# Kernel optimization log

Hardware: AMD Instinct MI355X
Metric: run time of the kernel (lower is better)

## Reference

```python
import jax, jax.numpy as jnp
import numpy as np

D_MODEL = 1024
N_HEADS = 16
EPS = 1e-6


def setup_inputs() -> dict:
    key = jax.random.key(0)
    k1, k2, k3 = jax.random.split(key, 3)
    B, T, D = 2, 2048, D_MODEL
    x = jax.random.normal(k1, (B, T, D), dtype=jnp.float32)
    # learned params
    norm_weight = jnp.ones((D,), dtype=jnp.float32)
    qkv_w = jax.random.normal(k2, (3 * D, D), dtype=jnp.float32) * (1.0 / np.sqrt(D))
    out_w = jax.random.normal(k3, (D, D), dtype=jnp.float32) * (1.0 / np.sqrt(D))
    return {"x": x, "norm_weight": norm_weight, "qkv_w": qkv_w, "out_w": out_w}


def reference(x, norm_weight, qkv_w, out_w):
    B, T, D = x.shape
    H = N_HEADS
    d = D // H
    # RMSNorm
    ms = jnp.mean(x * x, axis=-1, keepdims=True)
    xn = x * jax.lax.rsqrt(ms + EPS) * norm_weight
    # QKV projection (Linear, no bias): y = x @ W^T
    qkv = jnp.einsum('btd,ed->bte', xn, qkv_w)  # (B,T,3D)
    q, k, v = jnp.split(qkv, 3, axis=-1)
    q = q.reshape(B, T, H, d)
    k = k.reshape(B, T, H, d)
    v = v.reshape(B, T, H, d)
    # scores (B,H,T,T) with causal mask
    scores = jnp.einsum('bqhd,bkhd->bhqk', q, k) / np.sqrt(d).astype(np.float32)
    causal = jnp.tril(jnp.ones((T, T), dtype=bool))
    scores = jnp.where(causal[None, None], scores, -jnp.inf)
    probs = jax.nn.softmax(scores, axis=-1)
    ctx = jnp.einsum('bhqk,bkhd->bqhd', probs, v)  # (B,T,H,d)
    out = ctx.reshape(B, T, D)
    out = jnp.einsum('btd,ed->bte', out, out_w)
    return out
```

## Files before the change

kernel.cpp:

```cpp
#include <hip/hip_runtime.h>
#include <stdint.h>

#define B_SZ 2
#define T_SZ 2048
#define DMODEL 1024
#define HCNT 16
#define HD 64
#define MROWS (B_SZ * T_SZ)

typedef __attribute__((ext_vector_type(8))) __bf16 bf16x8;
typedef __attribute__((ext_vector_type(4))) __bf16 bf16x4;
typedef __attribute__((ext_vector_type(4))) float f32x4;
typedef __attribute__((ext_vector_type(8))) unsigned short u16x8;

__device__ __forceinline__ unsigned short f2bf(float f) {
  union { float f; uint32_t u; } v; v.f = f;
  uint32_t u = v.u;
  u += 0x7fffu + ((u >> 16) & 1u);
  return (unsigned short)(u >> 16);
}

__device__ __forceinline__ float fexp2(float x) {
#if __has_builtin(__builtin_amdgcn_exp2f)
  return __builtin_amdgcn_exp2f(x);
#else
  return exp2f(x);
#endif
}

__device__ __forceinline__ void gld_lds16(const void* g, void* l) {
  __builtin_amdgcn_global_load_lds((__attribute__((address_space(1))) void*)(uintptr_t)g,
                                   (__attribute__((address_space(3))) void*)l, 16, 0, 0);
}

__global__ __launch_bounds__(256)
void cvt_all(const float* __restrict__ qkv_w, const float* __restrict__ out_w,
             unsigned short* __restrict__ dst) {
  int i = blockIdx.x * 256 + threadIdx.x;
  const int n1 = 3 * DMODEL * DMODEL / 4;
  float4 v = (i < n1) ? ((const float4*)qkv_w)[i] : ((const float4*)out_w)[i - n1];
  ushort4 o;
  o.x = f2bf(v.x); o.y = f2bf(v.y); o.z = f2bf(v.z); o.w = f2bf(v.w);
  ((ushort4*)dst)[i] = o;
}

__global__ __launch_bounds__(256)
void rmsnorm_bf16(const float* __restrict__ x, const float* __restrict__ w,
                  unsigned short* __restrict__ xn) {
  const int row = blockIdx.x;
  const int t = threadIdx.x;
  float4 v = ((const float4*)(x + (size_t)row * DMODEL))[t];
  float ss = v.x * v.x + v.y * v.y + v.z * v.z + v.w * v.w;
#pragma unroll
  for (int o = 1; o < 64; o <<= 1) ss += __shfl_xor(ss, o, 64);
  __shared__ float red[4];
  if ((t & 63) == 0) red[t >> 6] = ss;
  __syncthreads();
  float tot = red[0] + red[1] + red[2] + red[3];
  float scale = rsqrtf(tot * (1.0f / (float)DMODEL) + 1e-6f);
  float4 wv = ((const float4*)w)[t];
  ushort4 o;
  o.x = f2bf(v.x * scale * wv.x);
  o.y = f2bf(v.y * scale * wv.y);
  o.z = f2bf(v.z * scale * wv.z);
  o.w = f2bf(v.w * scale * wv.w);
  ((ushort4*)(xn + (size_t)row * DMODEL))[t] = o;
}

__device__ __forceinline__ void stage128x32(const unsigned short* g, int ldg,
                                            unsigned short* lds, int wave, int lane) {
#pragma unroll
  for (int i = 0; i < 2; ++i) {
    const unsigned short* gp = g + (size_t)(i * 64 + wave * 16 + (lane >> 2)) * ldg + (lane & 3) * 8;
    gld_lds16(gp, lds + i * 2048 + wave * 512);
  }
}

template <int F32OUT>
__global__ __launch_bounds__(256, 2)
void gemm_bt(const unsigned short* __restrict__ A, const unsigned short* __restrict__ B,
             void* __restrict__ Cv, int M, int N, int K, int nbx) {
  __shared__ __align__(16) unsigned short As[2][128 * 32];
  __shared__ __align__(16) unsigned short Bs[2][128 * 32];
  const int t = threadIdx.x, wave = t >> 6, lane = t & 63;
  const int cpx = gridDim.x >> 3;
  const int swz = (blockIdx.x & 7) * cpx + (blockIdx.x >> 3);
  const int m0 = (swz / nbx) * 128, n0 = (swz % nbx) * 128;
  const int wr = wave >> 1, wc = wave & 1;
  f32x4 acc[4][4] = {};
  const int nk = K >> 5;
  stage128x32(A + (size_t)m0 * K, K, As[0], wave, lane);
  stage128x32(B + (size_t)n0 * K, K, Bs[0], wave, lane);
  __syncthreads();
  int buf = 0;
  for (int kt = 0; kt < nk; ++kt) {
    if (kt + 1 < nk) {
      stage128x32(A + (size_t)m0 * K + (kt + 1) * 32, K, As[buf ^ 1], wave, lane);
      stage128x32(B + (size_t)n0 * K + (kt + 1) * 32, K, Bs[buf ^ 1], wave, lane);
    }
    bf16x8 af[4], bfr[4];
#pragma unroll
    for (int mi = 0; mi < 4; ++mi)
      af[mi] = *(const bf16x8*)&As[buf][(wr * 64 + mi * 16 + (lane & 15)) * 32 + (lane >> 4) * 8];
#pragma unroll
    for (int ni = 0; ni < 4; ++ni)
      bfr[ni] = *(const bf16x8*)&Bs[buf][(wc * 64 + ni * 16 + (lane & 15)) * 32 + (lane >> 4) * 8];
#pragma unroll
    for (int mi = 0; mi < 4; ++mi)
#pragma unroll
      for (int ni = 0; ni < 4; ++ni)
        acc[mi][ni] = __builtin_amdgcn_mfma_f32_16x16x32_bf16(af[mi], bfr[ni], acc[mi][ni], 0, 0, 0);
    __syncthreads();
    buf ^= 1;
  }
  const int cr = (lane >> 4) * 4, cc = lane & 15;
#pragma unroll
  for (int mi = 0; mi < 4; ++mi)
#pragma unroll
    for (int ni = 0; ni < 4; ++ni) {
      int row = m0 + wr * 64 + mi * 16 + cr;
      int col = n0 + wc * 64 + ni * 16 + cc;
      if (F32OUT) {
        float* C = (float*)Cv;
#pragma unroll
        for (int r = 0; r < 4; ++r) C[(size_t)(row + r) * N + col] = acc[mi][ni][r];
      } else {
        unsigned short* C = (unsigned short*)Cv;
#pragma unroll
        for (int r = 0; r < 4; ++r) C[(size_t)(row + r) * N + col] = f2bf(acc[mi][ni][r]);
      }
    }
}

__global__ __launch_bounds__(256, 2)
void attn_causal(const unsigned short* __restrict__ qkv, unsigned short* __restrict__ ctx) {
  __shared__ __align__(16) unsigned short Ks[2][128 * 64];
  __shared__ __align__(16) unsigned short Vt[2][64 * 72];
  __shared__ __align__(16) unsigned short Pl[4][32 * 72];
  const int tid = threadIdx.x, wave = tid >> 6, lane = tid & 63;
  const int id = blockIdx.x;
  const int bh = (id & 7) + 8 * ((id >> 3) & 3);
  const int p = id >> 5;
  const int qt = (p < 8) ? (15 - p) : (p - 8);
  const int b = bh >> 4, h = bh & 15;
  const int q0 = qt * 128 + wave * 32;
  const size_t base = (size_t)b * T_SZ * 3 * DMODEL;
  const int koffK = DMODEL + h * HD;
  const int koffV = 2 * DMODEL + h * HD;
  const int nit = qt + 1;
  const int c = lane & 15, qg = lane >> 4;

  const float QSC = 0.125f * 1.4426950408889634f;
  bf16x8 aq[2][2];
#pragma unroll
  for (int mi = 0; mi < 2; ++mi)
#pragma unroll
    for (int kk = 0; kk < 2; ++kk) {
      int q = q0 + mi * 16 + c;
      bf16x8 f = *(const bf16x8*)(qkv + base + (size_t)q * 3 * DMODEL + h * HD + kk * 32 + qg * 8);
#pragma unroll
      for (int j = 0; j < 8; ++j) f[j] = (__bf16)((float)f[j] * QSC);
      aq[mi][kk] = f;
    }

  float mst[2] = {-3e38f, -3e38f}, lst[2] = {0.f, 0.f};
  f32x4 aco[2][4];
#pragma unroll
  for (int mi = 0; mi < 2; ++mi)
#pragma unroll
    for (int nd = 0; nd < 4; ++nd)
#pragma unroll
      for (int r = 0; r < 4; ++r) aco[mi][nd][r] = 0.f;

  const int kr = tid >> 3;
  const int kc = tid & 7;

  auto stageK = [&](int kb, int bufi) {
#pragma unroll
    for (int i = 0; i < 4; ++i) {
      int row = i * 32 + kr;
      gld_lds16(qkv + base + (size_t)(kb + row) * 3 * DMODEL + koffK + ((kc ^ (row & 7)) << 3),
                &Ks[bufi][i * 2048 + (wave << 9)]);
    }
  };
  auto loadV = [&](int kb, u16x8* v) {
#pragma unroll
    for (int i = 0; i < 4; ++i)
      v[i] = *(const u16x8*)(qkv + base + (size_t)(kb + i * 32 + kr) * 3 * DMODEL + koffV + kc * 8);
  };
  auto writeV = [&](const u16x8* v) {
#pragma unroll
    for (int i = 0; i < 4; ++i) {
      int ch = i >> 1;
      int kv = (i & 1) * 32 + kr;
#pragma unroll
      for (int j = 0; j < 8; ++j) {
        int dd = kc * 8 + j;
        int f = kc ^ j;
        Vt[ch][dd * 72 + ((((kv >> 3) ^ f) << 3) | (kv & 7))] = v[i][j];
      }
    }
  };

  auto computeTile = [&](int kb, int kbuf) {
    f32x4 s[8][2] = {};
    __builtin_amdgcn_s_setprio(1);
#pragma unroll
    for (int kk = 0; kk < 2; ++kk) {
      bf16x8 bk[8];
#pragma unroll
      for (int ni = 0; ni < 8; ++ni) {
        int row = ni * 16 + c;
        int crd = kk * 4 + qg;
        bk[ni] = *(const bf16x8*)&Ks[kbuf][row * 64 + ((crd ^ (row & 7)) << 3)];
      }
#pragma unroll
      for (int ni = 0; ni < 8; ++ni)
#pragma unroll
        for (int mi = 0; mi < 2; ++mi)
          s[ni][mi] = __builtin_amdgcn_mfma_f32_16x16x32_bf16(bk[ni], aq[mi][kk], s[ni][mi], 0, 0, 0);
    }
    __builtin_amdgcn_s_setprio(0);
    if (kb + 127 > q0) {
#pragma unroll
      for (int ni = 0; ni < 8; ++ni)
#pragma unroll
        for (int mi = 0; mi < 2; ++mi)
#pragma unroll
          for (int r = 0; r < 4; ++r) {
            int kg = kb + ni * 16 + qg * 4 + r;
            int qq = q0 + mi * 16 + c;
            if (kg > qq) s[ni][mi][r] = -1e30f;
          }
    }
#pragma unroll
    for (int mi = 0; mi < 2; ++mi) {
      float rm = -3e38f;
#pragma unroll
      for (int ni = 0; ni < 8; ++ni)
#pragma unroll
        for (int r = 0; r < 4; ++r) rm = fmaxf(rm, s[ni][mi][r]);
      rm = fmaxf(rm, __shfl_xor(rm, 16, 64));
      rm = fmaxf(rm, __shfl_xor(rm, 32, 64));
      float mo = mst[mi];
      float mn = mo;
      if (__any(rm > mo + 11.5f)) {
        mn = fmaxf(mo, rm);
        float corr = fexp2(mo - mn);
        lst[mi] *= corr;
        mst[mi] = mn;
#pragma unroll
        for (int r = 0; r < 4; ++r) {
          float cr = __shfl(corr, qg * 20 + r, 64);
#pragma unroll
          for (int nd = 0; nd < 4; ++nd) aco[mi][nd][r] *= cr;
        }
      }
      float rs = 0.f;
#pragma unroll
      for (int ni = 0; ni < 8; ++ni)
#pragma unroll
        for (int r = 0; r < 4; ++r) {
          float pv = fexp2(s[ni][mi][r] - mn);
          s[ni][mi][r] = pv;
          rs += pv;
        }
      rs += __shfl_xor(rs, 16, 64);
      rs += __shfl_xor(rs, 32, 64);
      lst[mi] += rs;
    }
    unsigned short* P = Pl[wave];
#pragma unroll
    for (int ch = 0; ch < 2; ++ch) {
      if (ch == 1) {
        asm volatile("s_waitcnt lgkmcnt(0)" ::: "memory");
        __builtin_amdgcn_sched_barrier(0);
      }
#pragma unroll
      for (int n2 = 0; n2 < 4; ++n2) {
        int ni = ch * 4 + n2;
#pragma unroll
        for (int mi = 0; mi < 2; ++mi) {
          bf16x4 pk;
#pragma unroll
          for (int r = 0; r < 4; ++r) pk[r] = (__bf16)s[ni][mi][r];
          *(bf16x4*)&P[(mi * 16 + c) * 72 + n2 * 16 + qg * 4] = pk;
        }
      }
      __builtin_amdgcn_s_setprio(1);
#pragma unroll
      for (int kk = 0; kk < 2; ++kk) {
        bf16x8 pa[2], bv[4];
#pragma unroll
        for (int mi = 0; mi < 2; ++mi)
          pa[mi] = *(const bf16x8*)&P[(mi * 16 + c) * 72 + kk * 32 + qg * 8];
#pragma unroll
        for (int nd = 0; nd < 4; ++nd) {
          int dd = nd * 16 + c;
          int f = ((dd >> 3) ^ dd) & 7;
          int crd = kk * 4 + qg;
          bv[nd] = *(const bf16x8*)&Vt[ch][dd * 72 + ((crd ^ f) << 3)];
        }
#pragma unroll
        for (int mi = 0; mi < 2; ++mi)
#pragma unroll
          for (int nd = 0; nd < 4; ++nd)
            aco[mi][nd] = __builtin_amdgcn_mfma_f32_16x16x32_bf16(pa[mi], bv[nd], aco[mi][nd], 0, 0, 0);
      }
      __builtin_amdgcn_s_setprio(0);
    }
  };

  stageK(0, 0);
  u16x8 v0[4];
  loadV(0, v0);
  __syncthreads();
  writeV(v0);
  __syncthreads();
  int kbuf = 0;
  for (int t = 0; t < nit; ++t) {
    const int kb = t * 128;
    const bool hn = (t + 1 < nit);
    u16x8 vn[4];
    if (hn) { stageK(kb + 128, kbuf ^ 1); loadV(kb + 128, vn); }
    computeTile(kb, kbuf);
    __syncthreads();
    if (hn) writeV(vn);
    __syncthreads();
    kbuf ^= 1;
  }

  unsigned short* outp = ctx + (size_t)b * T_SZ * DMODEL + h * HD;
#pragma unroll
  for (int mi = 0; mi < 2; ++mi) {
    float linv = 1.f / lst[mi];
#pragma unroll
    for (int r = 0; r < 4; ++r) {
      float inv = __shfl(linv, qg * 20 + r, 64);
      int q = q0 + mi * 16 + qg * 4 + r;
#pragma unroll
      for (int nd = 0; nd < 4; ++nd)
        outp[(size_t)q * DMODEL + nd * 16 + c] = f2bf(aco[mi][nd][r] * inv);
    }
  }
}

extern "C" void kernel_launch(void* const* d_in, const int* in_sizes, int n_in,
                              void* d_out, int out_size, void* d_ws, size_t ws_size,
                              hipStream_t stream) {
  const float* x = (const float*)d_in[0];
  const float* nw = (const float*)d_in[1];
  const float* qkv_w = (const float*)d_in[2];
  const float* out_w = (const float*)d_in[3];
  float* out = (float*)d_out;

  unsigned short* ws = (unsigned short*)d_ws;
  unsigned short* xn = ws;
  unsigned short* qkvw = xn + (size_t)MROWS * DMODEL;
  unsigned short* outw = qkvw + (size_t)3 * DMODEL * DMODEL;
  unsigned short* qkv = outw + (size_t)DMODEL * DMODEL;
  unsigned short* ctx = qkv + (size_t)MROWS * 3 * DMODEL;

  cvt_all<<<dim3(4096), dim3(256), 0, stream>>>(qkv_w, out_w, qkvw);
  rmsnorm_bf16<<<dim3(MROWS), dim3(256), 0, stream>>>(x, nw, xn);
  gemm_bt<0><<<dim3(768), dim3(256), 0, stream>>>(xn, qkvw, qkv, MROWS, 3 * DMODEL, DMODEL, 24);
  attn_causal<<<dim3(512), dim3(256), 0, stream>>>(qkv, ctx);
  gemm_bt<1><<<dim3(256), dim3(256), 0, stream>>>(ctx, outw, out, MROWS, DMODEL, DMODEL, 8);
}
```

Before: 121.1 us.

## Pair causal query tiles per attention block and widen GEMM K-tile

The attention kernel now launches 256 blocks of 512 threads. Each block handles two query tiles, p and 15-p, for one batch-head, so every block does a balanced amount of causal work and shares its K/V staging across both tiles. Each wave now owns 16 rows from each tile. V is double-buffered in LDS, which drops one barrier per iteration, and the two masked diagonal tiles are handled separately. Separately, the GEMM stages a 64-wide K slice per iteration to halve its loop trips and barriers, at the cost of double the LDS.

```diff
diff --git a/kernel.cpp b/kernel.cpp
--- a/kernel.cpp
+++ b/kernel.cpp
@@ -67,11 +67,12 @@
   ((ushort4*)(xn + (size_t)row * DMODEL))[t] = o;
 }
 
-__device__ __forceinline__ void stage128x32(const unsigned short* g, int ldg,
-                                            unsigned short* lds, int wave, int lane) {
-#pragma unroll
-  for (int i = 0; i < 2; ++i) {
-    const unsigned short* gp = g + (size_t)(i * 64 + wave * 16 + (lane >> 2)) * ldg + (lane & 3) * 8;
+__device__ __forceinline__ void stage128x64(const unsigned short* g, int ldg,
+                                            unsigned short* lds, int tid) {
+  const int wave = tid >> 6;
+#pragma unroll
+  for (int i = 0; i < 4; ++i) {
+    const unsigned short* gp = g + (size_t)(i * 32 + (tid >> 3)) * ldg + (tid & 7) * 8;
     gld_lds16(gp, lds + i * 2048 + wave * 512);
   }
 }
@@ -80,46 +81,50 @@
 __global__ __launch_bounds__(256, 2)
 void gemm_bt(const unsigned short* __restrict__ A, const unsigned short* __restrict__ B,
              void* __restrict__ Cv, int M, int N, int K, int nbx) {
-  __shared__ __align__(16) unsigned short As[2][128 * 32];
-  __shared__ __align__(16) unsigned short Bs[2][128 * 32];
+  __shared__ __align__(16) unsigned short As[2][128 * 64];
+  __shared__ __align__(16) unsigned short Bs[2][128 * 64];
   const int t = threadIdx.x, wave = t >> 6, lane = t & 63;
   const int cpx = gridDim.x >> 3;
   const int swz = (blockIdx.x & 7) * cpx + (blockIdx.x >> 3);
   const int m0 = (swz / nbx) * 128, n0 = (swz % nbx) * 128;
   const int wr = wave >> 1, wc = wave & 1;
+  const int c = lane & 15, qg = lane >> 4;
   f32x4 acc[4][4] = {};
-  const int nk = K >> 5;
-  stage128x32(A + (size_t)m0 * K, K, As[0], wave, lane);
-  stage128x32(B + (size_t)n0 * K, K, Bs[0], wave, lane);
+  const int nk = K >> 6;
+  stage128x64(A + (size_t)m0 * K, K, As[0], t);
+  stage128x64(B + (size_t)n0 * K, K, Bs[0], t);
   __syncthreads();
   int buf = 0;
   for (int kt = 0; kt < nk; ++kt) {
     if (kt + 1 < nk) {
-      stage128x32(A + (size_t)m0 * K + (kt + 1) * 32, K, As[buf ^ 1], wave, lane);
-      stage128x32(B + (size_t)n0 * K + (kt + 1) * 32, K, Bs[buf ^ 1], wave, lane);
-    }
-    bf16x8 af[4], bfr[4];
-#pragma unroll
-    for (int mi = 0; mi < 4; ++mi)
-      af[mi] = *(const bf16x8*)&As[buf][(wr * 64 + mi * 16 + (lane & 15)) * 32 + (lane >> 4) * 8];
-#pragma unroll
-    for (int ni = 0; ni < 4; ++ni)
-      bfr[ni] = *(const bf16x8*)&Bs[buf][(wc * 64 + ni * 16 + (lane & 15)) * 32 + (lane >> 4) * 8];
-#pragma unroll
-    for (int mi = 0; mi < 4; ++mi)
+      stage128x64(A + (size_t)m0 * K + (kt + 1) * 64, K, As[buf ^ 1], t);
+      stage128x64(B + (size_t)n0 * K + (kt + 1) * 64, K, Bs[buf ^ 1], t);
+    }
+#pragma unroll
+    for (int kk = 0; kk < 2; ++kk) {
+      bf16x8 af[4], bfr[4];
+#pragma unroll
+      for (int mi = 0; mi < 4; ++mi)
+        af[mi] = *(const bf16x8*)&As[buf][(wr * 64 + mi * 16 + c) * 64 + kk * 32 + qg * 8];
 #pragma unroll
       for (int ni = 0; ni < 4; ++ni)
-        acc[mi][ni] = __builtin_amdgcn_mfma_f32_16x16x32_bf16(af[mi], bfr[ni], acc[mi][ni], 0, 0, 0);
+        bfr[ni] = *(const bf16x8*)&Bs[buf][(wc * 64 + ni * 16 + c) * 64 + kk * 32 + qg * 8];
+#pragma unroll
+      for (int mi = 0; mi < 4; ++mi)
+#pragma unroll
+        for (int ni = 0; ni < 4; ++ni)
+          acc[mi][ni] = __builtin_amdgcn_mfma_f32_16x16x32_bf16(af[mi], bfr[ni], acc[mi][ni], 0, 0, 0);
+    }
     __syncthreads();
     buf ^= 1;
   }
-  const int cr = (lane >> 4) * 4, cc = lane & 15;
+  const int cr = qg * 4;
 #pragma unroll
   for (int mi = 0; mi < 4; ++mi)
 #pragma unroll
     for (int ni = 0; ni < 4; ++ni) {
       int row = m0 + wr * 64 + mi * 16 + cr;
-      int col = n0 + wc * 64 + ni * 16 + cc;
+      int col = n0 + wc * 64 + ni * 16 + c;
       if (F32OUT) {
         float* C = (float*)Cv;
 #pragma unroll
@@ -132,23 +137,23 @@
     }
 }
 
-__global__ __launch_bounds__(256, 2)
+__global__ __launch_bounds__(512, 2)
 void attn_causal(const unsigned short* __restrict__ qkv, unsigned short* __restrict__ ctx) {
   __shared__ __align__(16) unsigned short Ks[2][128 * 64];
-  __shared__ __align__(16) unsigned short Vt[2][64 * 72];
-  __shared__ __align__(16) unsigned short Pl[4][32 * 72];
+  __shared__ __align__(16) unsigned short Vt[2][2][64 * 72];
+  __shared__ __align__(16) unsigned short Pl[8][32 * 136];
   const int tid = threadIdx.x, wave = tid >> 6, lane = tid & 63;
   const int id = blockIdx.x;
-  const int bh = (id & 7) + 8 * ((id >> 3) & 3);
-  const int p = id >> 5;
-  const int qt = (p < 8) ? (15 - p) : (p - 8);
+  const int bh = (id & 7) | ((id >> 6) << 3);
+  const int p = (id >> 3) & 7;
   const int b = bh >> 4, h = bh & 15;
-  const int q0 = qt * 128 + wave * 32;
+  const int q0a = p * 128 + wave * 16;
+  const int q0b = (15 - p) * 128 + wave * 16;
+  const int nit = 16 - p;
+  const int c = lane & 15, qg = lane >> 4;
   const size_t base = (size_t)b * T_SZ * 3 * DMODEL;
   const int koffK = DMODEL + h * HD;
   const int koffV = 2 * DMODEL + h * HD;
-  const int nit = qt + 1;
-  const int c = lane & 15, qg = lane >> 4;
 
   const float QSC = 0.125f * 1.4426950408889634f;
   bf16x8 aq[2][2];
@@ -156,7 +161,7 @@
   for (int mi = 0; mi < 2; ++mi)
 #pragma unroll
     for (int kk = 0; kk < 2; ++kk) {
-      int q = q0 + mi * 16 + c;
+      int q = (mi ? q0b : q0a) + c;
       bf16x8 f = *(const bf16x8*)(qkv + base + (size_t)q * 3 * DMODEL + h * HD + kk * 32 + qg * 8);
 #pragma unroll
       for (int j = 0; j < 8; ++j) f[j] = (__bf16)((float)f[j] * QSC);
@@ -172,37 +177,69 @@
 #pragma unroll
       for (int r = 0; r < 4; ++r) aco[mi][nd][r] = 0.f;
 
-  const int kr = tid >> 3;
-  const int kc = tid & 7;
-
   auto stageK = [&](int kb, int bufi) {
 #pragma unroll
-    for (int i = 0; i < 4; ++i) {
-      int row = i * 32 + kr;
-      gld_lds16(qkv + base + (size_t)(kb + row) * 3 * DMODEL + koffK + ((kc ^ (row & 7)) << 3),
-                &Ks[bufi][i * 2048 + (wave << 9)]);
+    for (int i = 0; i < 2; ++i) {
+      int row = i * 64 + (tid >> 3);
+      gld_lds16(qkv + base + (size_t)(kb + row) * 3 * DMODEL + koffK + (((tid & 7) ^ (row & 7)) << 3),
+                &Ks[bufi][i * 4096 + (wave << 9)]);
     }
   };
   auto loadV = [&](int kb, u16x8* v) {
 #pragma unroll
-    for (int i = 0; i < 4; ++i)
-      v[i] = *(const u16x8*)(qkv + base + (size_t)(kb + i * 32 + kr) * 3 * DMODEL + koffV + kc * 8);
-  };
-  auto writeV = [&](const u16x8* v) {
-#pragma unroll
-    for (int i = 0; i < 4; ++i) {
-      int ch = i >> 1;
-      int kv = (i & 1) * 32 + kr;
+    for (int i = 0; i < 2; ++i)
+      v[i] = *(const u16x8*)(qkv + base + (size_t)(kb + i * 64 + (tid >> 3)) * 3 * DMODEL + koffV + (tid & 7) * 8);
+  };
+  auto writeV = [&](int bufi, const u16x8* v) {
+#pragma unroll
+    for (int i = 0; i < 2; ++i) {
+      int kv = tid >> 3;
 #pragma unroll
       for (int j = 0; j < 8; ++j) {
-        int dd = kc * 8 + j;
-        int f = kc ^ j;
-        Vt[ch][dd * 72 + ((((kv >> 3) ^ f) << 3) | (kv & 7))] = v[i][j];
-      }
-    }
-  };
-
-  auto computeTile = [&](int kb, int kbuf) {
+        int dd = (tid & 7) * 8 + j;
+        int f = (tid & 7) ^ j;
+        Vt[bufi][i][dd * 72 + ((((kv >> 3) ^ f) << 3) | (kv & 7))] = v[i][j];
+      }
+    }
+  };
+
+  auto softmaxRow = [&](int mi, f32x4 s[8][2]) {
+    float rm = -3e38f;
+#pragma unroll
+    for (int ni = 0; ni < 8; ++ni)
+#pragma unroll
+      for (int r = 0; r < 4; ++r) rm = fmaxf(rm, s[ni][mi][r]);
+    rm = fmaxf(rm, __shfl_xor(rm, 16, 64));
+    rm = fmaxf(rm, __shfl_xor(rm, 32, 64));
+    float mo = mst[mi];
+    float mn = mo;
+    if (__any(rm > mo + 11.5f)) {
+      mn = fmaxf(mo, rm);
+      float corr = fexp2(mo - mn);
+      lst[mi] *= corr;
+      mst[mi] = mn;
+#pragma unroll
+      for (int r = 0; r < 4; ++r) {
+        float cr = __shfl(corr, qg * 20 + r, 64);
+#pragma unroll
+        for (int nd = 0; nd < 4; ++nd) aco[mi][nd][r] *= cr;
+      }
+    }
+    float rs = 0.f;
+#pragma unroll
+    for (int ni = 0; ni < 8; ++ni)
+#pragma unroll
+      for (int r = 0; r < 4; ++r) {
+        float pv = fexp2(s[ni][mi][r] - mn);
+        s[ni][mi][r] = pv;
+        rs += pv;
+      }
+    rs += __shfl_xor(rs, 16, 64);
+    rs += __shfl_xor(rs, 32, 64);
+    lst[mi] += rs;
+  };
+
+  auto computeTile = [&](int kb, int kbuf, bool both, bool maskA, bool maskB) {
     f32x4 s[8][2] = {};
     __builtin_amdgcn_s_setprio(1);
 #pragma unroll
@@ -216,116 +253,91 @@
       }
 #pragma unroll
       for (int ni = 0; ni < 8; ++ni)
-#pragma unroll
-        for (int mi = 0; mi < 2; ++mi)
-          s[ni][mi] = __builtin_amdgcn_mfma_f32_16x16x32_bf16(bk[ni], aq[mi][kk], s[ni][mi], 0, 0, 0);
+        s[ni][1] = __builtin_amdgcn_mfma_f32_16x16x32_bf16(bk[ni], aq[1][kk], s[ni][1], 0, 0, 0);
+      if (both)
+#pragma unroll
+        for (int ni = 0; ni < 8; ++ni)
+          s[ni][0] = __builtin_amdgcn_mfma_f32_16x16x32_bf16(bk[ni], aq[0][kk], s[ni][0], 0, 0, 0);
     }
     __builtin_amdgcn_s_setprio(0);
-    if (kb + 127 > q0) {
+    if (maskB) {
 #pragma unroll
       for (int ni = 0; ni < 8; ++ni)
 #pragma unroll
-        for (int mi = 0; mi < 2; ++mi)
-#pragma unroll
-          for (int r = 0; r < 4; ++r) {
-            int kg = kb + ni * 16 + qg * 4 + r;
-            int qq = q0 + mi * 16 + c;
-            if (kg > qq) s[ni][mi][r] = -1e30f;
-          }
-    }
-#pragma unroll
-    for (int mi = 0; mi < 2; ++mi) {
-      float rm = -3e38f;
+        for (int r = 0; r < 4; ++r) {
+          int kg = kb + ni * 16 + qg * 4 + r;
+          if (kg > q0b + c) s[ni][1][r] = -1e30f;
+        }
+    }
+    if (both && maskA) {
 #pragma unroll
       for (int ni = 0; ni < 8; ++ni)
 #pragma unroll
-        for (int r = 0; r < 4; ++r) rm = fmaxf(rm, s[ni][mi][r]);
-      rm = fmaxf(rm, __shfl_xor(rm, 16, 64));
-      rm = fmaxf(rm, __shfl_xor(rm, 32, 64));
-      float mo = mst[mi];
-      float mn = mo;
-      if (__any(rm > mo + 11.5f)) {
-        mn = fmaxf(mo, rm);
-        float corr = fexp2(mo - mn);
-        lst[mi] *= corr;
-        mst[mi] = mn;
-#pragma unroll
         for (int r = 0; r < 4; ++r) {
-          float cr = __shfl(corr, qg * 20 + r, 64);
-#pragma unroll
-          for (int nd = 0; nd < 4; ++nd) aco[mi][nd][r] *= cr;
+          int kg = kb + ni * 16 + qg * 4 + r;
+          if (kg > q0a + c) s[ni][0][r] = -1e30f;
         }
-      }
-      float rs = 0.f;
-#pragma unroll
-      for (int ni = 0; ni < 8; ++ni)
-#pragma unroll
-        for (int r = 0; r < 4; ++r) {
-          float pv = fexp2(s[ni][mi][r] - mn);
-          s[ni][mi][r] = pv;
-          rs += pv;
-        }
-      rs += __shfl_xor(rs, 16, 64);
-      rs += __shfl_xor(rs, 32, 64);
-      lst[mi] += rs;
-    }
+    }
+    softmaxRow(1, s);
+    if (both) softmaxRow(0, s);
     unsigned short* P = Pl[wave];
 #pragma unroll
-    for (int ch = 0; ch < 2; ++ch) {
-      if (ch == 1) {
-        asm volatile("s_waitcnt lgkmcnt(0)" ::: "memory");
-        __builtin_amdgcn_sched_barrier(0);
-      }
-#pragma unroll
-      for (int n2 = 0; n2 < 4; ++n2) {
-        int ni = ch * 4 + n2;
-#pragma unroll
-        for (int mi = 0; mi < 2; ++mi) {
-          bf16x4 pk;
-#pragma unroll
-          for (int r = 0; r < 4; ++r) pk[r] = (__bf16)s[ni][mi][r];
-          *(bf16x4*)&P[(mi * 16 + c) * 72 + n2 * 16 + qg * 4] = pk;
-        }
-      }
-      __builtin_amdgcn_s_setprio(1);
+    for (int ni = 0; ni < 8; ++ni) {
+      {
+        bf16x4 pk;
+#pragma unroll
+        for (int r = 0; r < 4; ++r) pk[r] = (__bf16)s[ni][1][r];
+        *(bf16x4*)&P[(16 + c) * 136 + ni * 16 + qg * 4] = pk;
+      }
+      if (both) {
+        bf16x4 pk;
+#pragma unroll
+        for (int r = 0; r < 4; ++r) pk[r] = (__bf16)s[ni][0][r];
+        *(bf16x4*)&P[c * 136 + ni * 16 + qg * 4] = pk;
+      }
+    }
+    __builtin_amdgcn_s_setprio(1);
+#pragma unroll
+    for (int ch = 0; ch < 2; ++ch)
 #pragma unroll
       for (int kk = 0; kk < 2; ++kk) {
-        bf16x8 pa[2], bv[4];
-#pragma unroll
-        for (int mi = 0; mi < 2; ++mi)
-          pa[mi] = *(const bf16x8*)&P[(mi * 16 + c) * 72 + kk * 32 + qg * 8];
+        bf16x8 bv[4];
 #pragma unroll
         for (int nd = 0; nd < 4; ++nd) {
           int dd = nd * 16 + c;
           int f = ((dd >> 3) ^ dd) & 7;
           int crd = kk * 4 + qg;
-          bv[nd] = *(const bf16x8*)&Vt[ch][dd * 72 + ((crd ^ f) << 3)];
+          bv[nd] = *(const bf16x8*)&Vt[kbuf][ch][dd * 72 + ((crd ^ f) << 3)];
         }
-#pragma unroll
-        for (int mi = 0; mi < 2; ++mi)
+        bf16x8 pa1 = *(const bf16x8*)&P[(16 + c) * 136 + ch * 64 + kk * 32 + qg * 8];
+#pragma unroll
+        for (int nd = 0; nd < 4; ++nd)
+          aco[1][nd] = __builtin_amdgcn_mfma_f32_16x16x32_bf16(pa1, bv[nd], aco[1][nd], 0, 0, 0);
+        if (both) {
+          bf16x8 pa0 = *(const bf16x8*)&P[c * 136 + ch * 64 + kk * 32 + qg * 8];
 #pragma unroll
           for (int nd = 0; nd < 4; ++nd)
-            aco[mi][nd] = __builtin_amdgcn_mfma_f32_16x16x32_bf16(pa[mi], bv[nd], aco[mi][nd], 0, 0, 0);
-      }
-      __builtin_amdgcn_s_setprio(0);
-    }
+            aco[0][nd] = __builtin_amdgcn_mfma_f32_16x16x32_bf16(pa0, bv[nd], aco[0][nd], 0, 0, 0);
+        }
+      }
+    __builtin_amdgcn_s_setprio(0);
   };
 
   stageK(0, 0);
-  u16x8 v0[4];
-  loadV(0, v0);
-  __syncthreads();
-  writeV(v0);
+  {
+    u16x8 v0[2];
+    loadV(0, v0);
+    writeV(0, v0);
+  }
   __syncthreads();
   int kbuf = 0;
   for (int t = 0; t < nit; ++t) {
     const int kb = t * 128;
     const bool hn = (t + 1 < nit);
-    u16x8 vn[4];
+    u16x8 vn[2];
     if (hn) { stageK(kb + 128, kbuf ^ 1); loadV(kb + 128, vn); }
-    computeTile(kb, kbuf);
-    __syncthreads();
-    if (hn) writeV(vn);
+    computeTile(kb, kbuf, t <= p, t == p, t == nit - 1);
+    if (hn) writeV(kbuf ^ 1, vn);
     __syncthreads();
     kbuf ^= 1;
   }
@@ -337,7 +349,7 @@
 #pragma unroll
     for (int r = 0; r < 4; ++r) {
       float inv = __shfl(linv, qg * 20 + r, 64);
-      int q = q0 + mi * 16 + qg * 4 + r;
+      int q = (mi ? q0b : q0a) + qg * 4 + r;
 #pragma unroll
       for (int nd = 0; nd < 4; ++nd)
         outp[(size_t)q * DMODEL + nd * 16 + c] = f2bf(aco[mi][nd][r] * inv);
@@ -364,6 +376,6 @@
   cvt_all<<<dim3(4096), dim3(256), 0, stream>>>(qkv_w, out_w, qkvw);
   rmsnorm_bf16<<<dim3(MROWS), dim3(256), 0, stream>>>(x, nw, xn);
   gemm_bt<0><<<dim3(768), dim3(256), 0, stream>>>(xn, qkvw, qkv, MROWS, 3 * DMODEL, DMODEL, 24);
-  attn_causal<<<dim3(512), dim3(256), 0, stream>>>(qkv, ctx);
+  attn_causal<<<dim3(256), dim3(512), 0, stream>>>(qkv, ctx);
   gemm_bt<1><<<dim3(256), dim3(256), 0, stream>>>(ctx, outw, out, MROWS, DMODEL, DMODEL, 8);
 }
```

New measurement: 139.5 us. 1.15x slower.
